# Kernel optimization log

Measured on AMD Instinct MI355X. Metric: run time of the kernel, lower is better.

The kernel has to match this reference:

```python
import jax, jax.numpy as jnp
import numpy as np

B, S, D, H = 4, 1024, 1024, 16
DH = D // H  # head dim = 64


def setup_inputs() -> dict:
    key = jax.random.key(0)
    k0, k1, k2 = jax.random.split(key, 3)
    x = jax.random.normal(k0, (B, S, D), dtype=jnp.float32)
    c_attn_w = jax.random.normal(k1, (D, 3 * D), dtype=jnp.float32) * 0.02
    c_attn_b = jnp.zeros((3 * D,), dtype=jnp.float32)
    c_proj_w = jax.random.normal(k2, (D, D), dtype=jnp.float32) * 0.02
    c_proj_b = jnp.zeros((D,), dtype=jnp.float32)
    return {"x": x, "c_attn_w": c_attn_w, "c_attn_b": c_attn_b,
            "c_proj_w": c_proj_w, "c_proj_b": c_proj_b}


def reference(x, c_attn_w, c_attn_b, c_proj_w, c_proj_b):
    b, s, d = x.shape
    # Conv1D (GPT-2 style): out = x @ W + b, fused QKV
    qkv = jnp.einsum('bsd,de->bse', x, c_attn_w) + c_attn_b
    q, k, v = jnp.split(qkv, 3, axis=-1)
    # split heads -> [b, h, s, dh]
    q = q.reshape(b, s, H, DH).transpose(0, 2, 1, 3)
    k = k.reshape(b, s, H, DH).transpose(0, 2, 1, 3)
    v = v.reshape(b, s, H, DH).transpose(0, 2, 1, 3)
    # scaled scores with causal future mask (triu above diagonal -> -inf)
    w = jnp.einsum('bhqd,bhkd->bhqk', q, k) / jnp.sqrt(jnp.asarray(DH, x.dtype))
    future = jnp.triu(jnp.ones((s, s), dtype=bool), k=1)
    w = jnp.where(future[None, None, :, :], jnp.asarray(-jnp.inf, w.dtype), w)
    p = jax.nn.softmax(w, axis=-1)
    a = jnp.einsum('bhqk,bhkd->bhqd', p, v)
    # merge heads -> [b, s, d]
    a = a.transpose(0, 2, 1, 3).reshape(b, s, d)
    # output projection (Conv1D)
    out = jnp.einsum('bsd,de->bse', a, c_proj_w) + c_proj_b
    return out
```

## Files before the change

kernel.cpp:

```cpp
#include <hip/hip_runtime.h>
#include <math.h>

#define BB 4
#define SS 1024
#define DD 1024
#define HH 16
#define DHH 64

typedef short bf16x8 __attribute__((ext_vector_type(8)));
typedef float f32x4 __attribute__((ext_vector_type(4)));

__device__ __forceinline__ unsigned short f2bf(float f) {
    unsigned u = __float_as_uint(f);
    u += 0x7fffu + ((u >> 16) & 1u);
    return (unsigned short)(u >> 16);
}

__device__ __forceinline__ void glds16(const void* g, void* l) {
    __builtin_amdgcn_global_load_lds(
        (const __attribute__((address_space(1))) unsigned int*)g,
        (__attribute__((address_space(3))) unsigned int*)l, 16, 0, 0);
}

#define WAITCNT_VM(n)  (0xF70 | (n))
#define WAITCNT_LGKM0  (0xC07F)

__device__ __forceinline__ int swz(int row, int col) {
    return ((((col >> 4) ^ (row >> 2)) & 3) << 4) | (col & 15);
}

#define XCD_REMAP(flat, NWG) (((flat) & 7) * ((NWG) >> 3) + ((flat) >> 3))

__global__ __launch_bounds__(256) void prologue_kernel(
    const float* __restrict__ x, const float* __restrict__ w1,
    const float* __restrict__ w2, unsigned short* __restrict__ Xb,
    unsigned short* __restrict__ W1t, unsigned short* __restrict__ W2t)
{
    __shared__ float tile[64][65];
    const int bx = blockIdx.x;
    if (bx < 4096) {
        int i = bx * 256 + threadIdx.x;
        float4 v = ((const float4*)x)[i];
        ushort4 o = { f2bf(v.x), f2bf(v.y), f2bf(v.z), f2bf(v.w) };
        ((ushort4*)Xb)[i] = o;
        return;
    }
    const float* W; unsigned short* Wt; int N, n0, k0;
    if (bx < 4864) {
        int id = bx - 4096; W = w1; Wt = W1t; N = 3072;
        n0 = (id % 48) * 64; k0 = (id / 48) * 64;
    } else {
        int id = bx - 4864; W = w2; Wt = W2t; N = 1024;
        n0 = (id & 15) * 64; k0 = (id >> 4) * 64;
    }
    int c = threadIdx.x & 63, r0 = threadIdx.x >> 6;
    #pragma unroll
    for (int i = 0; i < 16; ++i) {
        int r = r0 + i * 4;
        tile[r][c] = W[(size_t)(k0 + r) * N + n0 + c];
    }
    __syncthreads();
    #pragma unroll
    for (int i = 0; i < 16; ++i) {
        int r = r0 + i * 4;
        Wt[(size_t)(n0 + r) * 1024 + k0 + c] = f2bf(tile[c][r]);
    }
}

__global__ __launch_bounds__(512, 2) void gemm_mfma(
    const unsigned short* __restrict__ A,
    const unsigned short* __restrict__ Bt,
    const float* __restrict__ bias,
    unsigned short* __restrict__ Cout,
    unsigned short* __restrict__ Vt,
    int N, int K)
{
    __shared__ unsigned short smem[65536];

    const int t = threadIdx.x;
    const int lane = t & 63;
    const int w = t >> 6;
    const int l15 = lane & 15, quad = lane >> 4;
    const int wr = w >> 2, wc = w & 3;

    const int flat = XCD_REMAP(blockIdx.y * 12 + blockIdx.x, 192);
    const int bm = (flat / 12) * 256, bn = (flat % 12) * 256;

    const int sl_ca = ((lane & 7) ^ (lane >> 3)) << 4;
    const unsigned short* sl_base =
        (sl_ca < 64) ? (A + (size_t)bm * K) : (Bt + (size_t)bn * K);
    const int sl_k = (sl_ca & 63) >> 1;

    auto stage = [&](int tile, int kh, int rh) {
        #pragma unroll
        for (int j = 0; j < 2; ++j) {
            int row = rh * 128 + j * 64 + w * 8 + (lane >> 3);
            glds16(sl_base + (size_t)row * K + tile * 64 + kh * 32 + sl_k,
                   &smem[((tile & 1) * 2 + kh) * 16384 +
                         rh * 8192 + j * 4096 + w * 512]);
        }
    };

    const f32x4 zero4 = {0.f, 0.f, 0.f, 0.f};
    f32x4 acc[8][4];
    #pragma unroll
    for (int i = 0; i < 8; ++i)
        #pragma unroll
        for (int j = 0; j < 4; ++j) acc[i][j] = zero4;

    const int T = K / 64;

    stage(0, 0, 0); stage(0, 0, 1); stage(0, 1, 0); stage(0, 1, 1);
    stage(1, 0, 0); stage(1, 0, 1);
    __builtin_amdgcn_s_waitcnt(WAITCNT_VM(4));

    bf16x8 bfr[4];
    for (int tt = 0; tt < T; ++tt) {
        const int buf = tt & 1;
        #pragma unroll
        for (int ph = 0; ph < 4; ++ph) {
            const int kh = ph >> 1;
            const int mh = ph & 1;
            __builtin_amdgcn_s_barrier();
            __builtin_amdgcn_sched_barrier(0);

            bf16x8 af[4];
            #pragma unroll
            for (int i = 0; i < 4; ++i) {
                int row = wr * 128 + (mh * 4 + i) * 16 + l15;
                int byte = (row << 7) + (quad << 4);
                byte ^= (l15 & 7) << 4;
                af[i] = *(const bf16x8*)&smem[(buf * 2 + kh) * 16384 + (byte >> 1)];
            }
            if (mh == 0) {
                #pragma unroll
                for (int nj = 0; nj < 4; ++nj) {
                    int row = wc * 64 + nj * 16 + l15;
                    int byte = (row << 7) + 64 + (quad << 4);
                    byte ^= (l15 & 7) << 4;
                    bfr[nj] = *(const bf16x8*)&smem[(buf * 2 + kh) * 16384 + (byte >> 1)];
                }
            }

            if (ph == 0)      { if (tt + 1 < T) stage(tt + 1, 1, 0); }
            else if (ph == 1) { if (tt + 1 < T) stage(tt + 1, 1, 1); }
            else if (ph == 2) { if (tt + 2 < T) stage(tt + 2, 0, 0); }
            else              { if (tt + 2 < T) stage(tt + 2, 0, 1); }

            __builtin_amdgcn_s_setprio(1);
            #pragma unroll
            for (int i = 0; i < 4; ++i)
                #pragma unroll
                for (int nj = 0; nj < 4; ++nj)
                    acc[mh * 4 + i][nj] = __builtin_amdgcn_mfma_f32_16x16x32_bf16(
                        af[i], bfr[nj], acc[mh * 4 + i][nj], 0, 0, 0);
            __builtin_amdgcn_s_setprio(0);

            __builtin_amdgcn_s_barrier();
        }
        if (tt + 2 < T)      __builtin_amdgcn_s_waitcnt(WAITCNT_VM(4));
        else if (tt + 1 < T) __builtin_amdgcn_s_waitcnt(WAITCNT_VM(0));
    }

    __syncthreads();

    float bv[4];
    #pragma unroll
    for (int nj = 0; nj < 4; ++nj) bv[nj] = bias[bn + wc * 64 + nj * 16 + l15];

    if (bn >= 2048) {
        #pragma unroll
        for (int mi = 0; mi < 8; ++mi)
            #pragma unroll
            for (int nj = 0; nj < 4; ++nj)
                #pragma unroll
                for (int r = 0; r < 4; ++r) {
                    int row = wr * 128 + mi * 16 + quad * 4 + r;
                    int col = wc * 64 + nj * 16 + l15;
                    smem[col * 256 + (row ^ (((col >> 2) & 3) << 4))] =
                        f2bf(acc[mi][nj][r] + bv[nj]);
                }
        __syncthreads();
        int b = bm >> 10, s0 = bm & 1023;
        int h0 = (bn - 2048) >> 6;
        #pragma unroll
        for (int it = 0; it < 16; ++it) {
            int chunk = it * 512 + t;
            int col = chunk >> 5;
            int r8 = (chunk & 31) * 8;
            bf16x8 val = *(const bf16x8*)&smem[col * 256 +
                         (r8 ^ (((col >> 2) & 3) << 4))];
            int h = h0 + (col >> 6), dh = col & 63;
            *(bf16x8*)&Vt[(((size_t)b * 16 + h) * 64 + dh) * 1024 + s0 + r8] = val;
        }
    } else {
        #pragma unroll
        for (int mi = 0; mi < 8; ++mi)
            #pragma unroll
            for (int nj = 0; nj < 4; ++nj)
                #pragma unroll
                for (int r = 0; r < 4; ++r) {
                    int row = wr * 128 + mi * 16 + quad * 4 + r;
                    int col = wc * 64 + nj * 16 + l15;
                    smem[row * 256 + (col ^ (((row >> 2) & 3) << 4))] =
                        f2bf(acc[mi][nj][r] + bv[nj]);
                }
        __syncthreads();
        #pragma unroll
        for (int it = 0; it < 16; ++it) {
            int chunk = it * 512 + t;
            int row = chunk >> 5;
            int col = (chunk & 31) * 8;
            bf16x8 val = *(const bf16x8*)&smem[row * 256 +
                         (col ^ (((row >> 2) & 3) << 4))];
            *(bf16x8*)&Cout[(size_t)(bm + row) * N + bn + col] = val;
        }
    }
}

__global__ __launch_bounds__(256) void gemm2_mfma(
    const unsigned short* __restrict__ A,
    const unsigned short* __restrict__ Bt,
    const float* __restrict__ bias,
    float* __restrict__ C,
    int N, int K)
{
    __shared__ unsigned short smem[18432];

    const int t = threadIdx.x;
    const int lane = t & 63;
    const int w = t >> 6;
    const int l15 = lane & 15, quad = lane >> 4;

    const int flat = XCD_REMAP(blockIdx.y * 8 + blockIdx.x, 512);
    const int bm = (flat / 8) * 64, bn = (flat % 8) * 128;

    const int fragoff = l15 * K + quad * 8;

    const f32x4 zero4 = {0.f, 0.f, 0.f, 0.f};
    f32x4 acc[2][4];
    #pragma unroll
    for (int i = 0; i < 2; ++i)
        #pragma unroll
        for (int j = 0; j < 4; ++j) acc[i][j] = zero4;

    const unsigned short* Abase = A  + (size_t)bm * K + fragoff;
    const unsigned short* Bbase = Bt + (size_t)bn * K + fragoff;

    const int R = K / 32;

    auto issue = [&](int k, int b) {
        glds16(Abase + (size_t)(w * 16) * K + k * 32,
               &smem[b * 6144 + w * 512]);
        #pragma unroll
        for (int g2 = 0; g2 < 2; ++g2) {
            int g = w * 2 + g2;
            glds16(Bbase + (size_t)(g * 16) * K + k * 32,
                   &smem[b * 6144 + 2048 + g * 512]);
        }
    };

    issue(0, 0);
    issue(1, 1);
    for (int k = 0; k < R; ++k) {
        if (k + 2 < R) {
            issue(k + 2, (k + 2) % 3);
            __builtin_amdgcn_s_waitcnt(WAITCNT_VM(6));
        } else if (k + 1 < R) {
            __builtin_amdgcn_s_waitcnt(WAITCNT_VM(3));
        } else {
            __builtin_amdgcn_s_waitcnt(WAITCNT_VM(0));
        }
        __builtin_amdgcn_s_barrier();

        bf16x8 af[2], bfr[4];
        #pragma unroll
        for (int mi = 0; mi < 2; ++mi)
            af[mi] = *(const bf16x8*)&smem[(k % 3) * 6144 + ((w >> 1) * 2 + mi) * 512 + lane * 8];
        #pragma unroll
        for (int nj = 0; nj < 4; ++nj)
            bfr[nj] = *(const bf16x8*)&smem[(k % 3) * 6144 + 2048 + ((w & 1) * 4 + nj) * 512 + lane * 8];
        #pragma unroll
        for (int mi = 0; mi < 2; ++mi)
            #pragma unroll
            for (int nj = 0; nj < 4; ++nj)
                acc[mi][nj] = __builtin_amdgcn_mfma_f32_16x16x32_bf16(
                    af[mi], bfr[nj], acc[mi][nj], 0, 0, 0);

        __builtin_amdgcn_s_barrier();
    }

    const int wm = (w >> 1) * 32;
    const int wn = (w & 1) * 64;
    float bv[4];
    #pragma unroll
    for (int nj = 0; nj < 4; ++nj) bv[nj] = bias[bn + wn + nj * 16 + l15];

    float* fs = (float*)smem;
    #pragma unroll
    for (int mi = 0; mi < 2; ++mi)
        #pragma unroll
        for (int nj = 0; nj < 4; ++nj)
            #pragma unroll
            for (int r = 0; r < 4; ++r)
                fs[(wm + mi * 16 + quad * 4 + r) * 128 + wn + nj * 16 + l15] =
                    acc[mi][nj][r] + bv[nj];
    __syncthreads();
    #pragma unroll
    for (int i = 0; i < 8; ++i) {
        int off = i * 256 + t;
        int row = off >> 5, col = (off & 31) * 4;
        *(float4*)&C[(size_t)(bm + row) * N + bn + col] =
            *(const float4*)&fs[row * 128 + col];
    }
}

__device__ __forceinline__ void attn_tile_step8(
    bf16x8 q0, bf16x8 q1, float* lsum, f32x4* o,
    const unsigned short (*Ks)[80], const unsigned short (*VsT)[80],
    unsigned short (*Ps)[80],
    int wq, int l15, int quad, bool diag)
{
    const f32x4 zero4 = {0.f, 0.f, 0.f, 0.f};
    f32x4 s[4];
    #pragma unroll
    for (int nj = 0; nj < 4; ++nj) {
        int n = nj * 16 + l15;
        f32x4 sa = zero4;
        bf16x8 b0 = *(const bf16x8*)&Ks[n][swz(n, quad * 8)];
        bf16x8 b1 = *(const bf16x8*)&Ks[n][swz(n, 32 + quad * 8)];
        sa = __builtin_amdgcn_mfma_f32_16x16x32_bf16(q0, b0, sa, 0, 0, 0);
        sa = __builtin_amdgcn_mfma_f32_16x16x32_bf16(q1, b1, sa, 0, 0, 0);
        s[nj] = sa;
    }
    const float scale = 0.125f;

    #pragma unroll
    for (int nj = 0; nj < 4; ++nj)
        #pragma unroll
        for (int r = 0; r < 4; ++r) {
            float sv = s[nj][r] * scale;
            if (diag && (nj * 16 + l15) > (wq * 16 + quad * 4 + r)) sv = -INFINITY;
            float p = __expf(sv);
            lsum[r] += p;
            int qloc = wq * 16 + quad * 4 + r;
            Ps[qloc][swz(qloc, nj * 16 + l15)] = f2bf(p);
        }

    #pragma unroll
    for (int kk = 0; kk < 2; ++kk) {
        int m = wq * 16 + l15;
        bf16x8 pa = *(const bf16x8*)&Ps[m][swz(m, kk * 32 + quad * 8)];
        #pragma unroll
        for (int nj = 0; nj < 4; ++nj) {
            int n = nj * 16 + l15;
            bf16x8 vb = *(const bf16x8*)&VsT[n][swz(n, kk * 32 + quad * 8)];
            o[nj] = __builtin_amdgcn_mfma_f32_16x16x32_bf16(pa, vb, o[nj], 0, 0, 0);
        }
    }
}

__global__ __launch_bounds__(512) void attn_mfma(
    const unsigned short* __restrict__ qkv,
    const unsigned short* __restrict__ Vt,
    unsigned short* __restrict__ aout)
{
    __shared__ unsigned short Ks[64][80];
    __shared__ unsigned short VsT[64][80];
    __shared__ unsigned short Ps[2][64][80];

    const int t = threadIdx.x;
    const int lane = t & 63;
    const int wave = t >> 6;
    const int wq = wave & 3;
    const int tile = wave >> 2;
    const int l15 = lane & 15, quad = lane >> 4;

    const int flat = XCD_REMAP(blockIdx.y * 8 + blockIdx.x, 512);
    const int qlo = flat % 8;
    const int bh = flat / 8;

    const int qhi = 15 - qlo;
    const int qb = tile ? qhi : qlo;
    const int b = bh >> 4, h = bh & 15;
    const size_t qkvbase = (size_t)b * SS * 3072;
    const f32x4 zero4 = {0.f, 0.f, 0.f, 0.f};

    bf16x8 qf0, qf1;
    {
        const unsigned short* p = qkv + qkvbase +
            (size_t)(qb * 64 + wq * 16 + l15) * 3072 + h * 64 + quad * 8;
        qf0 = *(const bf16x8*)p;
        qf1 = *(const bf16x8*)(p + 32);
    }

    float lsum[4];
    f32x4 o[4];
    #pragma unroll
    for (int r = 0; r < 4; ++r) lsum[r] = 0.f;
    #pragma unroll
    for (int nj = 0; nj < 4; ++nj) o[nj] = zero4;

    const int sr = t >> 3, scc = (t & 7) * 8;
    const unsigned short* kgp = qkv + qkvbase + 1024 + h * 64 + (size_t)sr * 3072 + scc;
    const unsigned short* vgp = Vt + ((size_t)bh * 64 + sr) * 1024 + scc;
    bf16x8 kreg, vreg;

    kreg = *(const bf16x8*)(kgp);
    vreg = *(const bf16x8*)(vgp);

    for (int kb = 0; kb <= qhi; ++kb) {
        __builtin_amdgcn_s_barrier();
        *(bf16x8*)&Ks[sr][swz(sr, scc)] = kreg;
        *(bf16x8*)&VsT[sr][swz(sr, scc)] = vreg;
        if (kb < qhi) {
            kreg = *(const bf16x8*)(kgp + (size_t)(kb + 1) * 64 * 3072);
            vreg = *(const bf16x8*)(vgp + (kb + 1) * 64);
        }
        __builtin_amdgcn_s_waitcnt(WAITCNT_LGKM0);
        __builtin_amdgcn_s_barrier();

        if (kb <= qb)
            attn_tile_step8(qf0, qf1, lsum, o, Ks, VsT, Ps[tile],
                            wq, l15, quad, kb == qb);
    }

    #pragma unroll
    for (int off = 1; off < 16; off <<= 1)
        #pragma unroll
        for (int r = 0; r < 4; ++r)
            lsum[r] += __shfl_xor(lsum[r], off);

    #pragma unroll
    for (int r = 0; r < 4; ++r) {
        float inv = 1.0f / lsum[r];
        int rloc = wq * 16 + quad * 4 + r;
        size_t ob = ((size_t)b * SS + qb * 64 + rloc) * 1024 + h * 64;
        #pragma unroll
        for (int nj = 0; nj < 4; ++nj)
            aout[ob + nj * 16 + l15] = f2bf(o[nj][r] * inv);
    }
}

extern "C" void kernel_launch(void* const* d_in, const int* in_sizes, int n_in,
                              void* d_out, int out_size, void* d_ws, size_t ws_size,
                              hipStream_t stream)
{
    const float* x     = (const float*)d_in[0];
    const float* wqkv  = (const float*)d_in[1];
    const float* bqkv  = (const float*)d_in[2];
    const float* wproj = (const float*)d_in[3];
    const float* bproj = (const float*)d_in[4];
    float* out = (float*)d_out;

    unsigned short* ws   = (unsigned short*)d_ws;
    unsigned short* Xb   = ws;
    unsigned short* W1t  = Xb  + (size_t)4096 * 1024;
    unsigned short* W2t  = W1t + (size_t)3072 * 1024;
    unsigned short* qkv  = W2t + (size_t)1024 * 1024;
    unsigned short* Vt   = qkv + (size_t)4096 * 3072;
    unsigned short* abuf = Vt  + (size_t)64 * 64 * 1024;

    prologue_kernel<<<5120, 256, 0, stream>>>(x, wqkv, wproj, Xb, W1t, W2t);

    gemm_mfma<<<dim3(3072 / 256, 4096 / 256), 512, 0, stream>>>(
        Xb, W1t, bqkv, qkv, Vt, 3072, 1024);

    attn_mfma<<<dim3(8, 64), 512, 0, stream>>>(qkv, Vt, abuf);

    gemm2_mfma<<<dim3(1024 / 128, 4096 / 64), 256, 0, stream>>>(
        abuf, W2t, bproj, out, 1024, 1024);
}
```

Measured before the change: 168.2 us.

## Retile QKV GEMM to 256x192 tiles so 256 blocks fill all CUs

Changes the fused QKV projection GEMM from 256x256 output tiles (192 blocks) to 256x192 tiles (256 blocks), so the grid matches the CU count and fewer CUs sit idle. The LDS staging is reorganised into separate A and B loaders with a paired-row swizzle, and B rows are clamped for the 192-wide tile. The epilogue is split three ways: pure Q/K tiles, pure V tiles that write transposed Vt, and one mixed tile that writes K columns to qkv and V head 0 to Vt. The narrower tile slightly lowers MFMA reuse per loaded byte and makes the epilogue more complex.

```diff
diff --git a/kernel.cpp b/kernel.cpp
--- a/kernel.cpp
+++ b/kernel.cpp
@@ -83,38 +83,48 @@
     const int l15 = lane & 15, quad = lane >> 4;
     const int wr = w >> 2, wc = w & 3;
 
-    const int flat = XCD_REMAP(blockIdx.y * 12 + blockIdx.x, 192);
-    const int bm = (flat / 12) * 256, bn = (flat % 12) * 256;
-
-    const int sl_ca = ((lane & 7) ^ (lane >> 3)) << 4;
-    const unsigned short* sl_base =
-        (sl_ca < 64) ? (A + (size_t)bm * K) : (Bt + (size_t)bn * K);
-    const int sl_k = (sl_ca & 63) >> 1;
-
-    auto stage = [&](int tile, int kh, int rh) {
-        #pragma unroll
-        for (int j = 0; j < 2; ++j) {
-            int row = rh * 128 + j * 64 + w * 8 + (lane >> 3);
-            glds16(sl_base + (size_t)row * K + tile * 64 + kh * 32 + sl_k,
-                   &smem[((tile & 1) * 2 + kh) * 16384 +
-                         rh * 8192 + j * 4096 + w * 512]);
-        }
+    const int flat = XCD_REMAP(blockIdx.y * 16 + blockIdx.x, 256);
+    const int tm = flat >> 4, tn = flat & 15;
+    const int bm = tm * 256, bn = tn * 192;
+
+    const int sl_ca  = ((lane & 7) ^ (lane >> 3)) << 4;
+    const int sl_odd = (sl_ca >= 64);
+    const int sl_k   = (sl_ca & 63) >> 1;
+    const int lane_pr = w * 8 + (lane >> 3);
+
+    const unsigned short* Asrc = A + (size_t)(bm + 2 * lane_pr + sl_odd) * K + sl_k;
+    const unsigned short* Bsrc0 = Bt + (size_t)(bn + 2 * lane_pr + sl_odd) * K + sl_k;
+    int brow1 = 128 + 2 * lane_pr + sl_odd;
+    if (brow1 > 191) brow1 = 191;
+    const unsigned short* Bsrc1 = Bt + (size_t)(bn + brow1) * K + sl_k;
+
+    auto stageA = [&](int tile, int kh) {
+        int toff = tile * 64 + kh * 32;
+        int dst = ((tile & 1) * 2 + kh) * 16384;
+        glds16(Asrc + toff,                    &smem[dst + w * 512]);
+        glds16(Asrc + (size_t)128 * K + toff,  &smem[dst + 4096 + w * 512]);
     };
+    auto stageB = [&](int tile, int kh) {
+        int toff = tile * 64 + kh * 32;
+        int dst = ((tile & 1) * 2 + kh) * 16384 + 8192;
+        glds16(Bsrc0 + toff, &smem[dst + w * 512]);
+        glds16(Bsrc1 + toff, &smem[dst + 4096 + w * 512]);
+    };
 
     const f32x4 zero4 = {0.f, 0.f, 0.f, 0.f};
-    f32x4 acc[8][4];
+    f32x4 acc[8][3];
     #pragma unroll
     for (int i = 0; i < 8; ++i)
         #pragma unroll
-        for (int j = 0; j < 4; ++j) acc[i][j] = zero4;
+        for (int j = 0; j < 3; ++j) acc[i][j] = zero4;
 
     const int T = K / 64;
 
-    stage(0, 0, 0); stage(0, 0, 1); stage(0, 1, 0); stage(0, 1, 1);
-    stage(1, 0, 0); stage(1, 0, 1);
+    stageA(0, 0); stageB(0, 0); stageA(0, 1); stageB(0, 1);
+    stageA(1, 0); stageB(1, 0);
     __builtin_amdgcn_s_waitcnt(WAITCNT_VM(4));
 
-    bf16x8 bfr[4];
+    bf16x8 bfr[3];
     for (int tt = 0; tt < T; ++tt) {
         const int buf = tt & 1;
         #pragma unroll
@@ -127,31 +137,31 @@
             bf16x8 af[4];
             #pragma unroll
             for (int i = 0; i < 4; ++i) {
-                int row = wr * 128 + (mh * 4 + i) * 16 + l15;
-                int byte = (row << 7) + (quad << 4);
-                byte ^= (l15 & 7) << 4;
+                int ar = wr * 128 + (mh * 4 + i) * 16 + l15;
+                int byte = (ar >> 1) * 128 + (ar & 1) * 64 + (quad << 4);
+                byte ^= ((ar >> 1) & 7) << 4;
                 af[i] = *(const bf16x8*)&smem[(buf * 2 + kh) * 16384 + (byte >> 1)];
             }
             if (mh == 0) {
                 #pragma unroll
-                for (int nj = 0; nj < 4; ++nj) {
-                    int row = wc * 64 + nj * 16 + l15;
-                    int byte = (row << 7) + 64 + (quad << 4);
-                    byte ^= (l15 & 7) << 4;
+                for (int nj = 0; nj < 3; ++nj) {
+                    int br = wc * 48 + nj * 16 + l15;
+                    int byte = 16384 + (br >> 1) * 128 + (br & 1) * 64 + (quad << 4);
+                    byte ^= ((br >> 1) & 7) << 4;
                     bfr[nj] = *(const bf16x8*)&smem[(buf * 2 + kh) * 16384 + (byte >> 1)];
                 }
             }
 
-            if (ph == 0)      { if (tt + 1 < T) stage(tt + 1, 1, 0); }
-            else if (ph == 1) { if (tt + 1 < T) stage(tt + 1, 1, 1); }
-            else if (ph == 2) { if (tt + 2 < T) stage(tt + 2, 0, 0); }
-            else              { if (tt + 2 < T) stage(tt + 2, 0, 1); }
+            if (ph == 0)      { if (tt + 1 < T) stageA(tt + 1, 1); }
+            else if (ph == 1) { if (tt + 1 < T) stageB(tt + 1, 1); }
+            else if (ph == 2) { if (tt + 2 < T) stageA(tt + 2, 0); }
+            else              { if (tt + 2 < T) stageB(tt + 2, 0); }
 
             __builtin_amdgcn_s_setprio(1);
             #pragma unroll
             for (int i = 0; i < 4; ++i)
                 #pragma unroll
-                for (int nj = 0; nj < 4; ++nj)
+                for (int nj = 0; nj < 3; ++nj)
                     acc[mh * 4 + i][nj] = __builtin_amdgcn_mfma_f32_16x16x32_bf16(
                         af[i], bfr[nj], acc[mh * 4 + i][nj], 0, 0, 0);
             __builtin_amdgcn_s_setprio(0);
@@ -164,27 +174,50 @@
 
     __syncthreads();
 
-    float bv[4];
-    #pragma unroll
-    for (int nj = 0; nj < 4; ++nj) bv[nj] = bias[bn + wc * 64 + nj * 16 + l15];
-
-    if (bn >= 2048) {
+    float bv[3];
+    #pragma unroll
+    for (int nj = 0; nj < 3; ++nj) bv[nj] = bias[bn + wc * 48 + nj * 16 + l15];
+
+    const int b = bm >> 10, s0 = bm & 1023;
+
+    if (tn <= 9) {
         #pragma unroll
         for (int mi = 0; mi < 8; ++mi)
             #pragma unroll
-            for (int nj = 0; nj < 4; ++nj)
+            for (int nj = 0; nj < 3; ++nj)
                 #pragma unroll
                 for (int r = 0; r < 4; ++r) {
                     int row = wr * 128 + mi * 16 + quad * 4 + r;
-                    int col = wc * 64 + nj * 16 + l15;
+                    int col = wc * 48 + nj * 16 + l15;
+                    smem[row * 192 + (col ^ (((row >> 2) & 3) << 4))] =
+                        f2bf(acc[mi][nj][r] + bv[nj]);
+                }
+        __syncthreads();
+        #pragma unroll
+        for (int it = 0; it < 12; ++it) {
+            int chunk = it * 512 + t;
+            int row = chunk / 24;
+            int col = (chunk % 24) * 8;
+            bf16x8 val = *(const bf16x8*)&smem[row * 192 +
+                         (col ^ (((row >> 2) & 3) << 4))];
+            *(bf16x8*)&Cout[(size_t)(bm + row) * N + bn + col] = val;
+        }
+    } else if (tn >= 11) {
+        #pragma unroll
+        for (int mi = 0; mi < 8; ++mi)
+            #pragma unroll
+            for (int nj = 0; nj < 3; ++nj)
+                #pragma unroll
+                for (int r = 0; r < 4; ++r) {
+                    int row = wr * 128 + mi * 16 + quad * 4 + r;
+                    int col = wc * 48 + nj * 16 + l15;
                     smem[col * 256 + (row ^ (((col >> 2) & 3) << 4))] =
                         f2bf(acc[mi][nj][r] + bv[nj]);
                 }
         __syncthreads();
-        int b = bm >> 10, s0 = bm & 1023;
         int h0 = (bn - 2048) >> 6;
         #pragma unroll
-        for (int it = 0; it < 16; ++it) {
+        for (int it = 0; it < 12; ++it) {
             int chunk = it * 512 + t;
             int col = chunk >> 5;
             int r8 = (chunk & 31) * 8;
@@ -197,23 +230,37 @@
         #pragma unroll
         for (int mi = 0; mi < 8; ++mi)
             #pragma unroll
-            for (int nj = 0; nj < 4; ++nj)
+            for (int nj = 0; nj < 3; ++nj)
                 #pragma unroll
                 for (int r = 0; r < 4; ++r) {
                     int row = wr * 128 + mi * 16 + quad * 4 + r;
-                    int col = wc * 64 + nj * 16 + l15;
-                    smem[row * 256 + (col ^ (((row >> 2) & 3) << 4))] =
-                        f2bf(acc[mi][nj][r] + bv[nj]);
+                    int col = wc * 48 + nj * 16 + l15;
+                    unsigned short v = f2bf(acc[mi][nj][r] + bv[nj]);
+                    if (col < 128)
+                        smem[row * 128 + (col ^ (((row >> 2) & 3) << 4))] = v;
+                    else {
+                        int vc = col - 128;
+                        smem[32768 + vc * 256 + (row ^ (((vc >> 2) & 3) << 4))] = v;
+                    }
                 }
         __syncthreads();
         #pragma unroll
-        for (int it = 0; it < 16; ++it) {
+        for (int it = 0; it < 8; ++it) {
             int chunk = it * 512 + t;
-            int row = chunk >> 5;
-            int col = (chunk & 31) * 8;
-            bf16x8 val = *(const bf16x8*)&smem[row * 256 +
+            int row = chunk >> 4;
+            int col = (chunk & 15) * 8;
+            bf16x8 val = *(const bf16x8*)&smem[row * 128 +
                          (col ^ (((row >> 2) & 3) << 4))];
             *(bf16x8*)&Cout[(size_t)(bm + row) * N + bn + col] = val;
+        }
+        #pragma unroll
+        for (int it = 0; it < 4; ++it) {
+            int chunk = it * 512 + t;
+            int vc = chunk >> 5;
+            int r8 = (chunk & 31) * 8;
+            bf16x8 val = *(const bf16x8*)&smem[32768 + vc * 256 +
+                         (r8 ^ (((vc >> 2) & 3) << 4))];
+            *(bf16x8*)&Vt[(((size_t)b * 16 + 0) * 64 + vc) * 1024 + s0 + r8] = val;
         }
     }
 }
@@ -463,7 +510,7 @@
 
     prologue_kernel<<<5120, 256, 0, stream>>>(x, wqkv, wproj, Xb, W1t, W2t);
 
-    gemm_mfma<<<dim3(3072 / 256, 4096 / 256), 512, 0, stream>>>(
+    gemm_mfma<<<dim3(16, 16), 512, 0, stream>>>(
         Xb, W1t, bqkv, qkv, Vt, 3072, 1024);
 
     attn_mfma<<<dim3(8, 64), 512, 0, stream>>>(qkv, Vt, abuf);
```

After: 164.5 us. -2.2%, faster.

## Double-buffer attention K/V tiles and use 512 threads in output GEMM

Applied to the files above, without the earlier changes.

The attention kernel now keeps two LDS buffers for K and V. The next tile is written to the spare buffer while the current one is computed, which removes one barrier per iteration and overlaps loads with MFMA work. The output projection GEMM moves from 4 to 8 waves per block, each wave covering a 32x32 sub-tile, with wait counts adjusted per wave. The trade-offs are more LDS per attention block and less work per wave in the GEMM.

```diff
diff --git a/kernel.cpp b/kernel.cpp
--- a/kernel.cpp
+++ b/kernel.cpp
@@ -218,7 +218,7 @@
     }
 }
 
-__global__ __launch_bounds__(256) void gemm2_mfma(
+__global__ __launch_bounds__(512) void gemm2_mfma(
     const unsigned short* __restrict__ A,
     const unsigned short* __restrict__ Bt,
     const float* __restrict__ bias,
@@ -238,11 +238,11 @@
     const int fragoff = l15 * K + quad * 8;
 
     const f32x4 zero4 = {0.f, 0.f, 0.f, 0.f};
-    f32x4 acc[2][4];
+    f32x4 acc[2][2];
     #pragma unroll
     for (int i = 0; i < 2; ++i)
         #pragma unroll
-        for (int j = 0; j < 4; ++j) acc[i][j] = zero4;
+        for (int j = 0; j < 2; ++j) acc[i][j] = zero4;
 
     const unsigned short* Abase = A  + (size_t)bm * K + fragoff;
     const unsigned short* Bbase = Bt + (size_t)bn * K + fragoff;
@@ -250,14 +250,11 @@
     const int R = K / 32;
 
     auto issue = [&](int k, int b) {
-        glds16(Abase + (size_t)(w * 16) * K + k * 32,
-               &smem[b * 6144 + w * 512]);
-        #pragma unroll
-        for (int g2 = 0; g2 < 2; ++g2) {
-            int g = w * 2 + g2;
-            glds16(Bbase + (size_t)(g * 16) * K + k * 32,
-                   &smem[b * 6144 + 2048 + g * 512]);
-        }
+        if (w < 4)
+            glds16(Abase + (size_t)(w * 16) * K + k * 32,
+                   &smem[b * 6144 + w * 512]);
+        glds16(Bbase + (size_t)(w * 16) * K + k * 32,
+               &smem[b * 6144 + 2048 + w * 512]);
     };
 
     issue(0, 0);
@@ -265,50 +262,52 @@
     for (int k = 0; k < R; ++k) {
         if (k + 2 < R) {
             issue(k + 2, (k + 2) % 3);
-            __builtin_amdgcn_s_waitcnt(WAITCNT_VM(6));
+            if (w < 4) __builtin_amdgcn_s_waitcnt(WAITCNT_VM(4));
+            else       __builtin_amdgcn_s_waitcnt(WAITCNT_VM(2));
         } else if (k + 1 < R) {
-            __builtin_amdgcn_s_waitcnt(WAITCNT_VM(3));
+            if (w < 4) __builtin_amdgcn_s_waitcnt(WAITCNT_VM(2));
+            else       __builtin_amdgcn_s_waitcnt(WAITCNT_VM(1));
         } else {
             __builtin_amdgcn_s_waitcnt(WAITCNT_VM(0));
         }
         __builtin_amdgcn_s_barrier();
 
-        bf16x8 af[2], bfr[4];
+        bf16x8 af[2], bfr[2];
         #pragma unroll
         for (int mi = 0; mi < 2; ++mi)
-            af[mi] = *(const bf16x8*)&smem[(k % 3) * 6144 + ((w >> 1) * 2 + mi) * 512 + lane * 8];
-        #pragma unroll
-        for (int nj = 0; nj < 4; ++nj)
-            bfr[nj] = *(const bf16x8*)&smem[(k % 3) * 6144 + 2048 + ((w & 1) * 4 + nj) * 512 + lane * 8];
+            af[mi] = *(const bf16x8*)&smem[(k % 3) * 6144 + ((w >> 2) * 2 + mi) * 512 + lane * 8];
+        #pragma unroll
+        for (int nj = 0; nj < 2; ++nj)
+            bfr[nj] = *(const bf16x8*)&smem[(k % 3) * 6144 + 2048 + ((w & 3) * 2 + nj) * 512 + lane * 8];
         #pragma unroll
         for (int mi = 0; mi < 2; ++mi)
             #pragma unroll
-            for (int nj = 0; nj < 4; ++nj)
+            for (int nj = 0; nj < 2; ++nj)
                 acc[mi][nj] = __builtin_amdgcn_mfma_f32_16x16x32_bf16(
                     af[mi], bfr[nj], acc[mi][nj], 0, 0, 0);
 
         __builtin_amdgcn_s_barrier();
     }
 
-    const int wm = (w >> 1) * 32;
-    const int wn = (w & 1) * 64;
-    float bv[4];
-    #pragma unroll
-    for (int nj = 0; nj < 4; ++nj) bv[nj] = bias[bn + wn + nj * 16 + l15];
+    const int wm = (w >> 2) * 32;
+    const int wn = (w & 3) * 32;
+    float bv[2];
+    #pragma unroll
+    for (int nj = 0; nj < 2; ++nj) bv[nj] = bias[bn + wn + nj * 16 + l15];
 
     float* fs = (float*)smem;
     #pragma unroll
     for (int mi = 0; mi < 2; ++mi)
         #pragma unroll
-        for (int nj = 0; nj < 4; ++nj)
+        for (int nj = 0; nj < 2; ++nj)
             #pragma unroll
             for (int r = 0; r < 4; ++r)
                 fs[(wm + mi * 16 + quad * 4 + r) * 128 + wn + nj * 16 + l15] =
                     acc[mi][nj][r] + bv[nj];
     __syncthreads();
     #pragma unroll
-    for (int i = 0; i < 8; ++i) {
-        int off = i * 256 + t;
+    for (int i = 0; i < 4; ++i) {
+        int off = i * 512 + t;
         int row = off >> 5, col = (off & 31) * 4;
         *(float4*)&C[(size_t)(bm + row) * N + bn + col] =
             *(const float4*)&fs[row * 128 + col];
@@ -365,8 +364,8 @@
     const unsigned short* __restrict__ Vt,
     unsigned short* __restrict__ aout)
 {
-    __shared__ unsigned short Ks[64][80];
-    __shared__ unsigned short VsT[64][80];
+    __shared__ unsigned short Ks[2][64][80];
+    __shared__ unsigned short VsT[2][64][80];
     __shared__ unsigned short Ps[2][64][80];
 
     const int t = threadIdx.x;
@@ -404,25 +403,33 @@
     const int sr = t >> 3, scc = (t & 7) * 8;
     const unsigned short* kgp = qkv + qkvbase + 1024 + h * 64 + (size_t)sr * 3072 + scc;
     const unsigned short* vgp = Vt + ((size_t)bh * 64 + sr) * 1024 + scc;
+    const int klds = swz(sr, scc);
     bf16x8 kreg, vreg;
 
     kreg = *(const bf16x8*)(kgp);
     vreg = *(const bf16x8*)(vgp);
+    *(bf16x8*)&Ks[0][sr][klds] = kreg;
+    *(bf16x8*)&VsT[0][sr][klds] = vreg;
+    kreg = *(const bf16x8*)(kgp + (size_t)64 * 3072);
+    vreg = *(const bf16x8*)(vgp + 64);
+    __builtin_amdgcn_s_waitcnt(WAITCNT_LGKM0);
+    __builtin_amdgcn_s_barrier();
 
     for (int kb = 0; kb <= qhi; ++kb) {
-        __builtin_amdgcn_s_barrier();
-        *(bf16x8*)&Ks[sr][swz(sr, scc)] = kreg;
-        *(bf16x8*)&VsT[sr][swz(sr, scc)] = vreg;
+        const int cur = kb & 1;
         if (kb < qhi) {
-            kreg = *(const bf16x8*)(kgp + (size_t)(kb + 1) * 64 * 3072);
-            vreg = *(const bf16x8*)(vgp + (kb + 1) * 64);
-        }
+            *(bf16x8*)&Ks[cur ^ 1][sr][klds] = kreg;
+            *(bf16x8*)&VsT[cur ^ 1][sr][klds] = vreg;
+            if (kb + 1 < qhi) {
+                kreg = *(const bf16x8*)(kgp + (size_t)(kb + 2) * 64 * 3072);
+                vreg = *(const bf16x8*)(vgp + (kb + 2) * 64);
+            }
+        }
+        if (kb <= qb)
+            attn_tile_step8(qf0, qf1, lsum, o, Ks[cur], VsT[cur], Ps[tile],
+                            wq, l15, quad, kb == qb);
         __builtin_amdgcn_s_waitcnt(WAITCNT_LGKM0);
         __builtin_amdgcn_s_barrier();
-
-        if (kb <= qb)
-            attn_tile_step8(qf0, qf1, lsum, o, Ks, VsT, Ps[tile],
-                            wq, l15, quad, kb == qb);
     }
 
     #pragma unroll
@@ -468,6 +475,6 @@
 
     attn_mfma<<<dim3(8, 64), 512, 0, stream>>>(qkv, Vt, abuf);
 
-    gemm2_mfma<<<dim3(1024 / 128, 4096 / 64), 256, 0, stream>>>(
+    gemm2_mfma<<<dim3(1024 / 128, 4096 / 64), 512, 0, stream>>>(
         abuf, W2t, bproj, out, 1024, 1024);
 }
```

New measurement: 168.5 us. No clear change (+0.1%).
